# Optimization experiments

Hardware: AMD Instinct MI355X
Metric: run time of the kernel (lower is better)

## Reference

```python
import jax, jax.numpy as jnp
import numpy as np

N_HEADS = 12
VAL_DIM = 64
TOKEN_DIM = 768


def setup_inputs() -> dict:
    key = jax.random.key(0)
    k1, k2, k3 = jax.random.split(key, 3)
    x = jax.random.normal(k1, (8, 1024, TOKEN_DIM), dtype=jnp.float32)
    W_qkv = jax.random.normal(k2, (TOKEN_DIM, 3 * N_HEADS * VAL_DIM), dtype=jnp.float32) * (TOKEN_DIM ** -0.5)
    W_merge = jax.random.normal(k3, (N_HEADS * VAL_DIM, TOKEN_DIM), dtype=jnp.float32) * ((N_HEADS * VAL_DIM) ** -0.5)
    return {"x": x, "W_qkv": W_qkv, "W_merge": W_merge}


def reference(x, W_qkv, W_merge):
    b, p, _ = x.shape
    scale = VAL_DIM ** -0.5
    qkv = jnp.einsum('bpt,tf->bpf', x, W_qkv)  # (b, p, 3*h*v)
    # einops '(h v k)' -> k is innermost factor
    qkv = qkv.reshape(b, p, N_HEADS, VAL_DIM, 3)
    q = jnp.transpose(qkv[..., 0], (0, 2, 1, 3))  # (b, h, p, v)
    k = jnp.transpose(qkv[..., 1], (0, 2, 1, 3))
    v = jnp.transpose(qkv[..., 2], (0, 2, 1, 3))
    scores = jnp.einsum('bhid,bhjd->bhij', q, k) * scale
    attn = jax.nn.softmax(scores, axis=-1)
    out = jnp.einsum('bhij,bhjd->bhid', attn, v)
    out = jnp.transpose(out, (0, 2, 1, 3)).reshape(b, p, N_HEADS * VAL_DIM)
    return jnp.einsum('bpf,ft->bpt', out, W_merge)
```

## Files before the change

kernel.cpp:

```cpp
#include <hip/hip_runtime.h>
#include <hip/hip_bf16.h>
#include <math.h>


#define B_  8
#define P_  1024
#define T_  768
#define H_  12
#define DV  64
#define F3  2304
#define HD  768
#define PSTR 72

typedef float  f32x4  __attribute__((ext_vector_type(4)));
typedef __bf16 bf16x4 __attribute__((ext_vector_type(4)));
typedef __bf16 bf16x8 __attribute__((ext_vector_type(8)));

#if defined(__has_builtin)
#if __has_builtin(__builtin_amdgcn_exp2f)
#define EX2(x) __builtin_amdgcn_exp2f(x)
#endif
#endif
#ifndef EX2
#define EX2(x) exp2f(x)
#endif

__device__ __forceinline__ void gload16(const void* g, void* l) {
    __builtin_amdgcn_global_load_lds((const __attribute__((address_space(1))) void*)g,
                                     (__attribute__((address_space(3))) void*)l,
                                     16, 0, 0);
}

__global__ __launch_bounds__(256) void k_cvt(const float* __restrict__ src,
                                             __bf16* __restrict__ dst) {
    int bid = blockIdx.x;
    int xcd = bid & 7;
    int seq = bid >> 3;
    int strip = (seq / 12) * 8 + xcd;
    int sub   = seq % 12;
    size_t base = (size_t)strip * (128 * T_) + (size_t)sub * (128 * T_ / 12);
    const float4* s4 = (const float4*)(src + base);
    bf16x4*       d4 = (bf16x4*)(dst + base);
#pragma unroll
    for (int i = 0; i < 8; i++) {
        float4 v = s4[i * 256 + threadIdx.x];
        bf16x4 o = { (__bf16)v.x, (__bf16)v.y, (__bf16)v.z, (__bf16)v.w };
        d4[i * 256 + threadIdx.x] = o;
    }
}

__global__ void k_tcvt(const float* __restrict__ src,
                       __bf16* __restrict__ dst, int R, int C) {
    __shared__ __bf16 tile[32][33];
    int tx = threadIdx.x, ty = threadIdx.y;
    int x = blockIdx.x * 32 + tx;
    int y = blockIdx.y * 32 + ty;
#pragma unroll
    for (int j = 0; j < 32; j += 8)
        tile[ty + j][tx] = (__bf16)src[(size_t)(y + j) * C + x];
    __syncthreads();
    int x2 = blockIdx.y * 32 + tx;
    int y2 = blockIdx.x * 32 + ty;
#pragma unroll
    for (int j = 0; j < 32; j += 8)
        dst[(size_t)(y2 + j) * R + x2] = tile[tx][ty + j];
}

__global__ void k_tcvt_qkv(const float* __restrict__ src,
                           __bf16* __restrict__ dst) {
    __shared__ __bf16 tile[32][33];
    int tx = threadIdx.x, ty = threadIdx.y;
    int n = blockIdx.x * 32 + tx;
    int r = n / 768, idx = n - r * 768;
    int f = (idx >> 6) * 192 + (idx & 63) * 3 + r;
    int t0 = blockIdx.y * 32;
#pragma unroll
    for (int j = 0; j < 32; j += 8)
        tile[ty + j][tx] = (__bf16)src[(size_t)(t0 + ty + j) * F3 + f];
    __syncthreads();
#pragma unroll
    for (int j = 0; j < 32; j += 8)
        dst[(size_t)(blockIdx.x * 32 + ty + j) * T_ + t0 + tx] = tile[tx][ty + j];
}

#define GEMM64_MAINLOOP(Aptr, Btptr, brow, bcol, LD)                             \
    int tid  = threadIdx.x;                                                      \
    int lane = tid & 63, wave = tid >> 6;                                        \
    int l16  = lane & 15, quad = lane >> 4;                                      \
    int wm = (wave >> 1) * 64, wn = (wave & 1) * 64;                             \
    int bro = tid >> 3, bq = tid & 7;                                            \
    f32x4 acc[4][4];                                                             \
    _Pragma("unroll") for (int i = 0; i < 4; i++)                                \
        _Pragma("unroll") for (int j = 0; j < 4; j++)                            \
            acc[i][j] = (f32x4){0.f, 0.f, 0.f, 0.f};                             \
    for (int k0 = 0; k0 < (LD); k0 += 64) {                                      \
        __syncthreads();                                                         \
        _Pragma("unroll") for (int it = 0; it < 4; it++) {                       \
            int n = it * 32 + bro;                                               \
            int gp = bq ^ (n & 7);                                               \
            gload16((Aptr) + (size_t)((brow) * 128 + n) * (LD) + k0 + gp * 8,    \
                    As + it * 2048 + tid * 8);                                   \
            gload16((Btptr) + (size_t)((bcol) * 128 + n) * (LD) + k0 + gp * 8,   \
                    Bs + it * 2048 + tid * 8);                                   \
        }                                                                        \
        __syncthreads();                                                         \
        _Pragma("unroll") for (int ks = 0; ks < 2; ks++) {                       \
            bf16x8 af[4], bfr[4];                                                \
            _Pragma("unroll") for (int i = 0; i < 4; i++) {                      \
                int r = wm + i * 16 + l16;                                       \
                af[i] = *(const bf16x8*)&As[r * 64 + (((ks * 4 + quad) ^ (r & 7)) << 3)]; \
            }                                                                    \
            _Pragma("unroll") for (int j = 0; j < 4; j++) {                      \
                int r = wn + j * 16 + l16;                                       \
                bfr[j] = *(const bf16x8*)&Bs[r * 64 + (((ks * 4 + quad) ^ (r & 7)) << 3)]; \
            }                                                                    \
            _Pragma("unroll") for (int i = 0; i < 4; i++)                        \
                _Pragma("unroll") for (int j = 0; j < 4; j++)                    \
                    acc[i][j] = __builtin_amdgcn_mfma_f32_16x16x32_bf16(         \
                        af[i], bfr[j], acc[i][j], 0, 0, 0);                      \
        }                                                                        \
    }

__global__ __launch_bounds__(256) void k_qkv(const __bf16* __restrict__ Xb,
                                             const __bf16* __restrict__ Wt,
                                             __bf16* __restrict__ Q,
                                             __bf16* __restrict__ K,
                                             __bf16* __restrict__ Vt) {
    __shared__ __align__(16) __bf16 LDSb[2 * 128 * 64];
    __bf16* As = LDSb;
    __bf16* Bs = LDSb + 128 * 64;

    int bid  = blockIdx.x;
    int xcd  = bid & 7;
    int seq  = bid >> 3;
    int brow = (seq / 18) * 8 + xcd;
    int bcol = seq % 18;

    GEMM64_MAINLOOP(Xb, Wt, brow, bcol, T_)

    int region = bcol / 6;
    int b  = brow >> 3;
    int p0 = (brow & 7) * 128;

    if (region < 2) {
        __bf16* D = region == 0 ? Q : K;
        float sc = region == 0 ? 0.1803368801f : 1.0f;
#pragma unroll
        for (int j = 0; j < 4; j++) {
            int idx = (bcol - region * 6) * 128 + wn + j * 16 + l16;
            int h = idx >> 6, v = idx & 63;
            __bf16* Dh = D + ((size_t)(b * H_ + h) * P_) * DV + v;
#pragma unroll
            for (int i = 0; i < 4; i++)
#pragma unroll
                for (int r = 0; r < 4; r++)
                    Dh[(size_t)(p0 + wm + i * 16 + quad * 4 + r) * DV] =
                        (__bf16)(acc[i][j][r] * sc);
        }
    } else {
        __syncthreads();
#pragma unroll
        for (int j = 0; j < 4; j++) {
            int n_loc = wn + j * 16 + l16;
#pragma unroll
            for (int i = 0; i < 4; i++)
#pragma unroll
            for (int r = 0; r < 4; r++) {
                int m_loc = wm + i * 16 + quad * 4 + r;
                int phys  = (m_loc >> 3) ^ (n_loc & 15);
                LDSb[n_loc * 128 + phys * 8 + (m_loc & 7)] = (__bf16)acc[i][j][r];
            }
        }
        __syncthreads();
        int n_loc = tid >> 1, halfm = tid & 1;
        int idx = (bcol - 12) * 128 + n_loc;
        int h = idx >> 6, v = idx & 63;
        __bf16* Dh = Vt + ((size_t)(b * H_ + h) * DV + v) * P_ + p0 + halfm * 64;
#pragma unroll
        for (int i = 0; i < 8; i++) {
            int chunk = halfm * 8 + i;
            int phys  = chunk ^ (n_loc & 15);
            bf16x8 val = *(const bf16x8*)&LDSb[n_loc * 128 + phys * 8];
            *(bf16x8*)(Dh + i * 8) = val;
        }
    }
}

__global__ __launch_bounds__(256) void k_merge(const __bf16* __restrict__ O,
                                               const __bf16* __restrict__ Wt,
                                               float* __restrict__ out) {
    __shared__ __align__(16) __bf16 LDSb[2 * 128 * 64];
    __bf16* As = LDSb;
    __bf16* Bs = LDSb + 128 * 64;

    int bid  = blockIdx.x;
    int xcd  = bid & 7;
    int seq  = bid >> 3;
    int brow = (seq / 6) * 8 + xcd;
    int bcol = seq % 6;

    GEMM64_MAINLOOP(O, Wt, brow, bcol, HD)

#pragma unroll
    for (int i = 0; i < 4; i++)
#pragma unroll
        for (int j = 0; j < 4; j++) {
            int col = bcol * 128 + wn + j * 16 + l16;
#pragma unroll
            for (int r = 0; r < 4; r++) {
                size_t row = (size_t)(brow * 128 + wm + i * 16 + quad * 4 + r);
                out[row * HD + col] = acc[i][j][r];
            }
        }
}

__global__ __launch_bounds__(256, 6) void k_attn(const __bf16* __restrict__ Q,
                                                 const __bf16* __restrict__ Kb,
                                                 const __bf16* __restrict__ Vt,
                                                 __bf16* __restrict__ O) {
    __shared__ __align__(16) __bf16 Ks[64 * 64];
    __shared__ __align__(16) __bf16 Vs[64 * 64];
    __shared__ __align__(16) __bf16 Pb[4][16 * PSTR];

    int tid  = threadIdx.x;
    int lane = tid & 63, wave = tid >> 6;
    int l16  = lane & 15, quad = lane >> 4;

    int bid = blockIdx.x;
    int xcd = bid & 7;
    int seq = bid >> 3;
    int bh  = xcd * 12 + (seq % 12);
    int qt  = seq / 12;
    int b   = bh / H_, h = bh % H_;

    const __bf16* Qb  = Q  + (size_t)bh * P_ * DV;
    const __bf16* Kbh = Kb + (size_t)bh * P_ * DV;
    const __bf16* Vbh = Vt + (size_t)bh * DV * P_;
    int m0 = qt * 64 + wave * 16;

    bf16x8 a0 = *(const bf16x8*)(Qb + (size_t)(m0 + l16) * DV + quad * 8);
    bf16x8 a1 = *(const bf16x8*)(Qb + (size_t)(m0 + l16) * DV + 32 + quad * 8);

    int l8 = lane >> 3, q8 = lane & 7;

    bf16x8 ones;
#pragma unroll
    for (int i = 0; i < 8; i++) ones[i] = (__bf16)1.0f;

    __bf16* Pw = &Pb[wave][0];
    f32x4 facc = {0.f, 0.f, 0.f, 0.f};
    f32x4 oacc[4] = {{0.f,0.f,0.f,0.f},{0.f,0.f,0.f,0.f},{0.f,0.f,0.f,0.f},{0.f,0.f,0.f,0.f}};
    int swq = l16 & 7;

    for (int c = 0; c < P_; c += 64) {
        __syncthreads();
#pragma unroll
        for (int i = 0; i < 2; i++) {
            int t = wave * 2 + i;
            int r = t * 8 + l8;
            int j = q8 ^ (r & 7);
            gload16(Kbh + (size_t)(c + r) * DV + j * 8, Ks + t * 512 + lane * 8);
            gload16(Vbh + (size_t)r * P_ + c + j * 8,  Vs + t * 512 + lane * 8);
        }
        __syncthreads();

        f32x4 s[4];
#pragma unroll
        for (int ct = 0; ct < 4; ct++) {
            int R = ct * 16 + l16;
            bf16x8 b0 = *(const bf16x8*)&Ks[R * 64 + ((quad ^ swq) * 8)];
            bf16x8 b1 = *(const bf16x8*)&Ks[R * 64 + (((4 + quad) ^ swq) * 8)];
            f32x4 z = {0.f, 0.f, 0.f, 0.f};
            z = __builtin_amdgcn_mfma_f32_16x16x32_bf16(b0, a0, z, 0, 0, 0);
            s[ct] = __builtin_amdgcn_mfma_f32_16x16x32_bf16(b1, a1, z, 0, 0, 0);
        }

#pragma unroll
        for (int ct = 0; ct < 4; ct++) {
            bf16x4 pk;
#pragma unroll
            for (int r = 0; r < 4; r++)
                pk[r] = (__bf16)EX2(s[ct][r]);
            *(bf16x4*)&Pw[l16 * PSTR + ct * 16 + quad * 4] = pk;
        }

#pragma unroll
        for (int ks = 0; ks < 2; ks++) {
            bf16x8 pfrag = *(const bf16x8*)&Pw[l16 * PSTR + ks * 32 + quad * 8];
            facc = __builtin_amdgcn_mfma_f32_16x16x32_bf16(ones, pfrag, facc, 0, 0, 0);
#pragma unroll
            for (int nt = 0; nt < 4; nt++) {
                int R = nt * 16 + l16;
                bf16x8 av = *(const bf16x8*)&Vs[R * 64 + (((ks * 4 + quad) ^ swq) * 8)];
                oacc[nt] = __builtin_amdgcn_mfma_f32_16x16x32_bf16(av, pfrag, oacc[nt], 0, 0, 0);
            }
        }
    }

    float inv = 1.0f / facc[0];

    int p = m0 + l16;
    __bf16* Orow = O + ((size_t)b * P_ + p) * HD + h * DV;
#pragma unroll
    for (int nt = 0; nt < 4; nt++) {
        bf16x4 o4;
#pragma unroll
        for (int r = 0; r < 4; r++) o4[r] = (__bf16)(oacc[nt][r] * inv);
        *(bf16x4*)&Orow[nt * 16 + quad * 4] = o4;
    }
}

extern "C" void kernel_launch(void* const* d_in, const int* in_sizes, int n_in,
                              void* d_out, int out_size, void* d_ws, size_t ws_size,
                              hipStream_t stream) {
    const float* x      = (const float*)d_in[0];
    const float* wqkv   = (const float*)d_in[1];
    const float* wmerge = (const float*)d_in[2];

    char* w = (char*)d_ws;
    __bf16* Xb  = (__bf16*)w;  w += (size_t)B_ * P_ * T_ * 2;
    __bf16* WqT = (__bf16*)w;  w += (size_t)F3 * T_ * 2;
    __bf16* WmT = (__bf16*)w;  w += (size_t)HD * T_ * 2;
    __bf16* Q   = (__bf16*)w;  w += (size_t)B_ * H_ * P_ * DV * 2;
    __bf16* K   = (__bf16*)w;  w += (size_t)B_ * H_ * P_ * DV * 2;
    __bf16* Vt  = (__bf16*)w;  w += (size_t)B_ * H_ * P_ * DV * 2;
    __bf16* O   = (__bf16*)w;

    hipLaunchKernelGGL(k_cvt, dim3(768), dim3(256), 0, stream, x, Xb);

    dim3 tb(32, 8);
    hipLaunchKernelGGL(k_tcvt_qkv, dim3(F3 / 32, T_ / 32), tb, 0, stream, wqkv, WqT);
    hipLaunchKernelGGL(k_tcvt,     dim3(HD / 32, T_ / 32), tb, 0, stream, wmerge, WmT, T_, HD);

    hipLaunchKernelGGL(k_qkv, dim3((B_ * P_ / 128) * (F3 / 128)), dim3(256), 0, stream,
                       Xb, WqT, Q, K, Vt);

    hipLaunchKernelGGL(k_attn, dim3(B_ * H_ * (P_ / 64)), dim3(256), 0, stream,
                       Q, K, Vt, O);

    hipLaunchKernelGGL(k_merge, dim3((B_ * P_ / 128) * (HD / 128)), dim3(256), 0, stream,
                       O, WmT, (float*)d_out);
}
```

Baseline: 192.3 us.

## Double-buffer LDS tiles in QKV and merge GEMM main loops

The GEMM main loop now prefetches the next K-slice of A and B into a second LDS buffer while MFMAs run on the current one, cutting one barrier per iteration. LDS per block doubles to 64KB and launch bounds request two blocks per CU. This targets global-load latency exposed between the load and compute phases, at the cost of less LDS headroom and possibly lower occupancy. The epilogues still reuse LDSb from offset zero after the loop's final barrier.

```diff
diff --git a/kernel.cpp b/kernel.cpp
--- a/kernel.cpp
+++ b/kernel.cpp
@@ -93,17 +93,30 @@
     _Pragma("unroll") for (int i = 0; i < 4; i++)                                \
         _Pragma("unroll") for (int j = 0; j < 4; j++)                            \
             acc[i][j] = (f32x4){0.f, 0.f, 0.f, 0.f};                             \
+    _Pragma("unroll") for (int it = 0; it < 4; it++) {                           \
+        int n = it * 32 + bro;                                                   \
+        int gp = bq ^ (n & 7);                                                   \
+        gload16((Aptr) + (size_t)((brow) * 128 + n) * (LD) + gp * 8,             \
+                LDSb + it * 2048 + tid * 8);                                     \
+        gload16((Btptr) + (size_t)((bcol) * 128 + n) * (LD) + gp * 8,            \
+                LDSb + 8192 + it * 2048 + tid * 8);                              \
+    }                                                                            \
+    __syncthreads();                                                             \
     for (int k0 = 0; k0 < (LD); k0 += 64) {                                      \
-        __syncthreads();                                                         \
-        _Pragma("unroll") for (int it = 0; it < 4; it++) {                       \
-            int n = it * 32 + bro;                                               \
-            int gp = bq ^ (n & 7);                                               \
-            gload16((Aptr) + (size_t)((brow) * 128 + n) * (LD) + k0 + gp * 8,    \
-                    As + it * 2048 + tid * 8);                                   \
-            gload16((Btptr) + (size_t)((bcol) * 128 + n) * (LD) + k0 + gp * 8,   \
-                    Bs + it * 2048 + tid * 8);                                   \
+        int cur = (k0 >> 6) & 1;                                                 \
+        __bf16* As = LDSb + cur * 16384;                                         \
+        __bf16* Bs = As + 8192;                                                  \
+        if (k0 + 64 < (LD)) {                                                    \
+            __bf16* Ad = LDSb + (cur ^ 1) * 16384;                               \
+            _Pragma("unroll") for (int it = 0; it < 4; it++) {                   \
+                int n = it * 32 + bro;                                           \
+                int gp = bq ^ (n & 7);                                           \
+                gload16((Aptr) + (size_t)((brow) * 128 + n) * (LD) + k0 + 64 + gp * 8, \
+                        Ad + it * 2048 + tid * 8);                               \
+                gload16((Btptr) + (size_t)((bcol) * 128 + n) * (LD) + k0 + 64 + gp * 8, \
+                        Ad + 8192 + it * 2048 + tid * 8);                        \
+            }                                                                    \
         }                                                                        \
-        __syncthreads();                                                         \
         _Pragma("unroll") for (int ks = 0; ks < 2; ks++) {                       \
             bf16x8 af[4], bfr[4];                                                \
             _Pragma("unroll") for (int i = 0; i < 4; i++) {                      \
@@ -119,16 +132,15 @@
                     acc[i][j] = __builtin_amdgcn_mfma_f32_16x16x32_bf16(         \
                         af[i], bfr[j], acc[i][j], 0, 0, 0);                      \
         }                                                                        \
-    }
-
-__global__ __launch_bounds__(256) void k_qkv(const __bf16* __restrict__ Xb,
-                                             const __bf16* __restrict__ Wt,
-                                             __bf16* __restrict__ Q,
-                                             __bf16* __restrict__ K,
-                                             __bf16* __restrict__ Vt) {
-    __shared__ __align__(16) __bf16 LDSb[2 * 128 * 64];
-    __bf16* As = LDSb;
-    __bf16* Bs = LDSb + 128 * 64;
+        __syncthreads();                                                         \
+    }
+
+__global__ __launch_bounds__(256, 2) void k_qkv(const __bf16* __restrict__ Xb,
+                                                const __bf16* __restrict__ Wt,
+                                                __bf16* __restrict__ Q,
+                                                __bf16* __restrict__ K,
+                                                __bf16* __restrict__ Vt) {
+    __shared__ __align__(16) __bf16 LDSb[2 * 2 * 128 * 64];
 
     int bid  = blockIdx.x;
     int xcd  = bid & 7;
@@ -186,12 +198,10 @@
     }
 }
 
-__global__ __launch_bounds__(256) void k_merge(const __bf16* __restrict__ O,
-                                               const __bf16* __restrict__ Wt,
-                                               float* __restrict__ out) {
-    __shared__ __align__(16) __bf16 LDSb[2 * 128 * 64];
-    __bf16* As = LDSb;
-    __bf16* Bs = LDSb + 128 * 64;
+__global__ __launch_bounds__(256, 2) void k_merge(const __bf16* __restrict__ O,
+                                                  const __bf16* __restrict__ Wt,
+                                                  float* __restrict__ out) {
+    __shared__ __align__(16) __bf16 LDSb[2 * 2 * 128 * 64];
 
     int bid  = blockIdx.x;
     int xcd  = bid & 7;
```

After: 183.0 us. -4.8%, faster.
